# Kernel optimization log

Hardware: AMD Instinct MI355X
Metric: run time of the kernel (lower is better)

Reference implementation:

```python
import jax, jax.numpy as jnp
import numpy as np

B, N, E, D = 32, 144, 127, 512   # batch, seq (forced to 144 by additive PE), embed_size, encoding_size
H, DK, DV = 8, 64, 64            # heads, dim_k, dim_v
F = 32 * D                       # forward_expansion=32 (default)
L = 4                            # num_layers
EPS = 1e-5


def setup_inputs() -> dict:
    key = jax.random.key(0)
    ks = jax.random.split(key, 20)
    s = 0.02
    x = jax.random.normal(ks[0], (B, N, E), jnp.float32)
    # causal mask: True = masked (future positions)
    future_mask = jnp.broadcast_to(jnp.triu(jnp.ones((N, N), bool), k=1), (B, N, N))
    inp = {
        'batch_size': B,
        'x': x,
        'future_mask': future_mask,
        'Wenc': jax.random.normal(ks[1], (E + 1, D), jnp.float32) * s,
        'benc': jnp.zeros((D,), jnp.float32),
        'Wq': jax.random.normal(ks[2], (L, D, H * DK), jnp.float32) * s,
        'Wk': jax.random.normal(ks[3], (L, D, H * DK), jnp.float32) * s,
        'Wv': jax.random.normal(ks[4], (L, D, H * DV), jnp.float32) * s,
        'Wo': jax.random.normal(ks[5], (L, H * DV, D), jnp.float32) * s,
        'bo': jnp.zeros((L, D), jnp.float32),
        'ln1_g': jnp.ones((L, D), jnp.float32), 'ln1_b': jnp.zeros((L, D), jnp.float32),
        'ln2_g': jnp.ones((L, D), jnp.float32), 'ln2_b': jnp.zeros((L, D), jnp.float32),
        'ln3_g': jnp.ones((L, D), jnp.float32), 'ln3_b': jnp.zeros((L, D), jnp.float32),
        'W1': jax.random.normal(ks[6], (L, D, F), jnp.float32) * s,
        'b1': jnp.zeros((L, F), jnp.float32),
        'W2': jax.random.normal(ks[7], (L, F, D), jnp.float32) * s,
        'b2': jnp.zeros((L, D), jnp.float32),
        'Wdec': jax.random.normal(ks[8], (D, E), jnp.float32) * s,
        'bdec': jnp.zeros((E,), jnp.float32),
    }
    return inp


def _layernorm(x, g, b):
    mu = jnp.mean(x, axis=-1, keepdims=True)
    var = jnp.var(x, axis=-1, keepdims=True)
    return (x - mu) * jax.lax.rsqrt(var + EPS) * g + b


def _mha(values_in, keys_in, query_in, mask, Wq, Wk, Wv, Wo, bo):
    b = query_in.shape[0]
    q = (query_in @ Wq).reshape(b, -1, H, DK).transpose(0, 2, 1, 3)   # [b,H,N,DK]
    k = (keys_in @ Wk).reshape(b, -1, H, DK).transpose(0, 2, 1, 3)
    v = (values_in @ Wv).reshape(b, -1, H, DV).transpose(0, 2, 1, 3)  # [b,H,N,DV]
    scores = jnp.einsum('bhnk,bhmk->bhnm', q, k)  # NOTE: no 1/sqrt(dk) scaling in original
    if mask is not None:
        scores = jnp.where(mask[:, None, :, :], jnp.float32(-1e20), scores)
    attn = jax.nn.softmax(scores, axis=-1)
    # torch.einsum('bhnn,bhnv->bhnv') takes the DIAGONAL of attn and scales v elementwise
    diag = jnp.diagonal(attn, axis1=2, axis2=3)  # [b,H,N]
    out = diag[..., None] * v                    # [b,H,N,DV]
    out = out.transpose(0, 2, 1, 3).reshape(b, -1, H * DV)
    return out @ Wo + bo


def reference(batch_size, x, future_mask, Wenc, benc, Wq, Wk, Wv, Wo, bo,
              ln1_g, ln1_b, ln2_g, ln2_b, ln3_g, ln3_b, W1, b1, W2, b2, Wdec, bdec):
    # Additive positional encoding: append arange(N)/max as extra channel
    pe = (jnp.arange(N, dtype=jnp.float32) / jnp.float32(N - 1))[None, :, None]
    xp = jnp.concatenate([x, jnp.broadcast_to(pe, (x.shape[0], N, 1))], axis=2)
    xe = xp @ Wenc + benc  # [B,N,D]
    out = xe
    for l in range(L):
        a = _mha(out, out, out, future_mask, Wq[l], Wk[l], Wv[l], Wo[l], bo[l])
        q = _layernorm(a + xe, ln1_g[l], ln1_b[l])
        a = _mha(xe, xe, q, None, Wq[l], Wk[l], Wv[l], Wo[l], bo[l])
        ff = jax.nn.relu(a @ W1[l] + b1[l]) @ W2[l] + b2[l]
        ao = _layernorm(ff + a, ln2_g[l], ln2_b[l])
        ff2 = jax.nn.relu(ao @ W1[l] + b1[l]) @ W2[l] + b2[l]
        out = _layernorm(ao + ff2, ln3_g[l], ln3_b[l])
    return out @ Wdec + bdec  # [B,N,E]
```

## Files before the change

### kernel.cpp

```cpp
#include <hip/hip_runtime.h>
#include <stdint.h>


typedef unsigned short u16;
typedef unsigned int   u32;
typedef __attribute__((ext_vector_type(8))) short s16x8;
typedef __attribute__((ext_vector_type(4))) float f32x4;

#define AS1 __attribute__((address_space(1)))
#define AS3 __attribute__((address_space(3)))

__device__ __forceinline__ float bf2f(u16 h) { return __uint_as_float(((u32)h) << 16); }
__device__ __forceinline__ u16 f2bf(float f) {
  u32 u = __float_as_uint(f);
  u32 r = (u + 0x7fffu + ((u >> 16) & 1u)) >> 16;
  return (u16)r;
}
__device__ __forceinline__ void gl_lds16(const u16* g, u16* l) {
  __builtin_amdgcn_global_load_lds((const AS1 void*)g, (AS3 void*)l, 16, 0, 0);
}

template<bool BIAS, bool RELU, bool OBF>
__global__ __launch_bounds__(256, 2)
void gemm_bt(const u16* __restrict__ A, int lda,
             const u16* __restrict__ Bt, int ldb,
             void* __restrict__ Cv, int ldc,
             const float* __restrict__ bias,
             int K, int nreal, long long sstride)
{
  __shared__ __align__(16) u16 As[2][128 * 64];
  __shared__ __align__(16) u16 Bs[2][128 * 64];
  const int tid  = threadIdx.x;
  const int wave = tid >> 6, lane = tid & 63;
  const int m0 = blockIdx.x * 128, n0 = blockIdx.y * 128;
  const long long koff = (long long)blockIdx.z * K;
  A  += (size_t)m0 * lda + koff;
  Bt += (size_t)n0 * ldb + koff;

  const int r0 = tid >> 3;
  const int sp = ((tid & 7) ^ (r0 & 7)) * 8;
  const u16* gA = A  + (size_t)r0 * lda + sp;
  const u16* gB = Bt + (size_t)r0 * ldb + sp;
  u16* lA = &As[0][tid * 8];
  u16* lB = &Bs[0][tid * 8];

  const int wr = (wave >> 1) * 64, wc = (wave & 1) * 64;
  const int fr = lane & 15, kq = lane >> 4;
  const int s0 = ((0 * 4 + kq) ^ (fr & 7)) * 8;
  const int s1 = ((1 * 4 + kq) ^ (fr & 7)) * 8;

  f32x4 acc[4][4] = {};
  const int NT = K >> 6;

#pragma unroll
  for (int q = 0; q < 4; ++q) gl_lds16(gA + (size_t)q * 32 * lda, lA + q * 2048);
#pragma unroll
  for (int q = 0; q < 4; ++q) gl_lds16(gB + (size_t)q * 32 * ldb, lB + q * 2048);
  gA += 64; gB += 64;

  for (int t = 0; t < NT; ++t) {
    __syncthreads();
    const int cur = t & 1;
    if (t + 1 < NT) {
      u16* dA = lA + (cur ^ 1) * (128 * 64);
      u16* dB = lB + (cur ^ 1) * (128 * 64);
#pragma unroll
      for (int q = 0; q < 4; ++q) gl_lds16(gA + (size_t)q * 32 * lda, dA + q * 2048);
#pragma unroll
      for (int q = 0; q < 4; ++q) gl_lds16(gB + (size_t)q * 32 * ldb, dB + q * 2048);
      gA += 64; gB += 64;
    }
    const u16* Ab = &As[cur][0];
    const u16* Bb = &Bs[cur][0];
    s16x8 a0[4], a1[4], b0[4], b1[4];
#pragma unroll
    for (int i = 0; i < 4; ++i) {
      const int ra = (wr + i * 16 + fr) * 64;
      a0[i] = *(const s16x8*)&Ab[ra + s0];
      a1[i] = *(const s16x8*)&Ab[ra + s1];
    }
#pragma unroll
    for (int j = 0; j < 4; ++j) {
      const int rb = (wc + j * 16 + fr) * 64;
      b0[j] = *(const s16x8*)&Bb[rb + s0];
      b1[j] = *(const s16x8*)&Bb[rb + s1];
    }
#pragma unroll
    for (int i = 0; i < 4; ++i)
#pragma unroll
      for (int j = 0; j < 4; ++j)
        acc[i][j] = __builtin_amdgcn_mfma_f32_16x16x32_bf16(a0[i], b0[j], acc[i][j], 0, 0, 0);
#pragma unroll
    for (int i = 0; i < 4; ++i)
#pragma unroll
      for (int j = 0; j < 4; ++j)
        acc[i][j] = __builtin_amdgcn_mfma_f32_16x16x32_bf16(a1[i], b1[j], acc[i][j], 0, 0, 0);
  }

#pragma unroll
  for (int j = 0; j < 4; ++j) {
    const int ccol = n0 + wc + j * 16 + fr;
    if (ccol >= nreal) continue;
    const float bv = BIAS ? bias[ccol] : 0.0f;
#pragma unroll
    for (int i = 0; i < 4; ++i) {
#pragma unroll
      for (int r = 0; r < 4; ++r) {
        const int crow = m0 + wr + i * 16 + kq * 4 + r;
        float v = acc[i][j][r] + bv;
        if (RELU) v = fmaxf(v, 0.0f);
        if (OBF) ((u16*)Cv)[(size_t)crow * ldc + ccol] = f2bf(v);
        else ((float*)Cv + (size_t)blockIdx.z * sstride)[(size_t)crow * ldc + ccol] = v;
      }
    }
  }
}

__global__ void tcvt(u16* __restrict__ Wt, const float* __restrict__ W,
                     int K, int N, int Npad)
{
  __shared__ float t[32][33];
  const int n0 = blockIdx.x * 32, k0 = blockIdx.y * 32;
  const int tx = threadIdx.x, ty = threadIdx.y;
#pragma unroll
  for (int i = 0; i < 4; ++i) {
    int k = k0 + ty + i * 8, n = n0 + tx;
    t[ty + i * 8][tx] = (k < K && n < N) ? W[(size_t)k * N + n] : 0.f;
  }
  __syncthreads();
#pragma unroll
  for (int i = 0; i < 4; ++i) {
    int n = n0 + ty + i * 8, k = k0 + tx;
    if (n < Npad) Wt[(size_t)n * K + k] = f2bf(t[tx][ty + i * 8]);
  }
}

template<bool CAUSAL>
__global__ __launch_bounds__(192)
void attn_diag(float* __restrict__ diag,
               const u16* __restrict__ Q, int ldq,
               const u16* __restrict__ Kp, int ldk)
{
  __shared__ float Kl[144][64];
  const int bh = blockIdx.x;
  const int b = bh >> 3, h = bh & 7;
  const int tid = threadIdx.x;

  for (int c = tid; c < 144 * 8; c += 192) {
    int m = c >> 3, c8 = c & 7;
    uint4 u = *(const uint4*)(Kp + (size_t)(b * 144 + m) * ldk + h * 64 + c8 * 8);
    float* dst = &Kl[m][c8 * 8];
    dst[0] = __uint_as_float(u.x << 16); dst[1] = __uint_as_float(u.x & 0xffff0000u);
    dst[2] = __uint_as_float(u.y << 16); dst[3] = __uint_as_float(u.y & 0xffff0000u);
    dst[4] = __uint_as_float(u.z << 16); dst[5] = __uint_as_float(u.z & 0xffff0000u);
    dst[6] = __uint_as_float(u.w << 16); dst[7] = __uint_as_float(u.w & 0xffff0000u);
  }
  __syncthreads();
  if (tid >= 144) return;
  const int n = tid;
  float q[64];
  const uint4* qp = (const uint4*)(Q + (size_t)(b * 144 + n) * ldq + h * 64);
#pragma unroll
  for (int c = 0; c < 8; ++c) {
    uint4 u = qp[c];
    q[c*8+0] = __uint_as_float(u.x << 16); q[c*8+1] = __uint_as_float(u.x & 0xffff0000u);
    q[c*8+2] = __uint_as_float(u.y << 16); q[c*8+3] = __uint_as_float(u.y & 0xffff0000u);
    q[c*8+4] = __uint_as_float(u.z << 16); q[c*8+5] = __uint_as_float(u.z & 0xffff0000u);
    q[c*8+6] = __uint_as_float(u.w << 16); q[c*8+7] = __uint_as_float(u.w & 0xffff0000u);
  }
  const int mmax = CAUSAL ? n : 143;
  float mx = -3.4e38f, sm = 0.f, sdiag = 0.f;
  for (int m = 0; m <= mmax; ++m) {
    float s0 = 0, s1 = 0, s2 = 0, s3 = 0;
#pragma unroll
    for (int c = 0; c < 64; c += 4) {
      s0 = fmaf(q[c + 0], Kl[m][c + 0], s0);
      s1 = fmaf(q[c + 1], Kl[m][c + 1], s1);
      s2 = fmaf(q[c + 2], Kl[m][c + 2], s2);
      s3 = fmaf(q[c + 3], Kl[m][c + 3], s3);
    }
    float s = (s0 + s1) + (s2 + s3);
    if (m == n) sdiag = s;
    float nmx = fmaxf(mx, s);
    sm = sm * __expf(mx - nmx) + __expf(s - nmx);
    mx = nmx;
  }
  diag[(size_t)bh * 144 + n] = __expf(sdiag - mx) / sm;
}

__global__ void scale_v(u16* __restrict__ outb, const float* __restrict__ diag,
                        const u16* __restrict__ V, int ldv)
{
  const int idx = blockIdx.x * 256 + threadIdx.x;
  const int r = idx >> 9, d = idx & 511;
  const int b = r / 144, n = r - b * 144;
  const int h = d >> 6;
  const float dg = diag[((size_t)b * 8 + h) * 144 + n];
  outb[(size_t)r * 512 + d] = f2bf(dg * bf2f(V[(size_t)r * ldv + d]));
}

__global__ __launch_bounds__(128)
void ln_dual(float* __restrict__ outf, u16* __restrict__ outb,
             const float* __restrict__ A, const float* __restrict__ Bv,
             const float* __restrict__ g, const float* __restrict__ be)
{
  const int r = blockIdx.x, t = threadIdx.x;
  float4 a = ((const float4*)(A + (size_t)r * 512))[t];
  float4 b = ((const float4*)(Bv + (size_t)r * 512))[t];
  const float x0 = a.x + b.x, x1 = a.y + b.y, x2 = a.z + b.z, x3 = a.w + b.w;
  float s = x0 + x1 + x2 + x3;
  float q = x0 * x0 + x1 * x1 + x2 * x2 + x3 * x3;
#pragma unroll
  for (int off = 32; off > 0; off >>= 1) { s += __shfl_down(s, off); q += __shfl_down(q, off); }
  __shared__ float ss[2], qs[2];
  if ((t & 63) == 0) { ss[t >> 6] = s; qs[t >> 6] = q; }
  __syncthreads();
  s = ss[0] + ss[1]; q = qs[0] + qs[1];
  const float mean = s * (1.f / 512.f);
  const float var  = q * (1.f / 512.f) - mean * mean;
  const float rs = rsqrtf(var + 1e-5f);
  float4 gg = ((const float4*)g)[t];
  float4 bb = ((const float4*)be)[t];
  const float o0 = (x0 - mean) * rs * gg.x + bb.x;
  const float o1 = (x1 - mean) * rs * gg.y + bb.y;
  const float o2 = (x2 - mean) * rs * gg.z + bb.z;
  const float o3 = (x3 - mean) * rs * gg.w + bb.w;
  if (outf) ((float4*)(outf + (size_t)r * 512))[t] = make_float4(o0, o1, o2, o3);
  if (outb) {
    uint2 u;
    u.x = (u32)f2bf(o0) | ((u32)f2bf(o1) << 16);
    u.y = (u32)f2bf(o2) | ((u32)f2bf(o3) << 16);
    ((uint2*)(outb + (size_t)r * 512))[t] = u;
  }
}

__global__ void f32_to_bf16_vec(u16* __restrict__ o, const float* __restrict__ a)
{
  const int i = blockIdx.x * 256 + threadIdx.x;
  float4 v = ((const float4*)a)[i];
  uint2 u;
  u.x = (u32)f2bf(v.x) | ((u32)f2bf(v.y) << 16);
  u.y = (u32)f2bf(v.z) | ((u32)f2bf(v.w) << 16);
  ((uint2*)o)[i] = u;
}

__global__ void reduce_ff(float* __restrict__ ff, const float* __restrict__ parts,
                          const float* __restrict__ bias)
{
  const int i = blockIdx.x * 256 + threadIdx.x;
  float4 acc = ((const float4*)bias)[i & 127];
#pragma unroll
  for (int s = 0; s < 8; ++s) {
    float4 p = ((const float4*)(parts + (size_t)s * 4608 * 512))[i];
    acc.x += p.x; acc.y += p.y; acc.z += p.z; acc.w += p.w;
  }
  ((float4*)ff)[i] = acc;
}

__global__ void build_xp(u16* __restrict__ xp, const float* __restrict__ x)
{
  const int i = blockIdx.x * 256 + threadIdx.x;
  const int r = i >> 7, e = i & 127;
  const float v = (e < 127) ? x[(size_t)r * 127 + e] : (float)(r % 144) * (1.f / 143.f);
  xp[i] = f2bf(v);
}

extern "C" void kernel_launch(void* const* d_in, const int* in_sizes, int n_in,
                              void* d_out, int out_size, void* d_ws, size_t ws_size,
                              hipStream_t stream)
{
  (void)in_sizes; (void)n_in; (void)out_size; (void)ws_size;
  const float* x    = (const float*)d_in[1];
  const float* Wenc = (const float*)d_in[3];
  const float* benc = (const float*)d_in[4];
  const float* Wq   = (const float*)d_in[5];
  const float* Wk   = (const float*)d_in[6];
  const float* Wv   = (const float*)d_in[7];
  const float* Wo   = (const float*)d_in[8];
  const float* bo   = (const float*)d_in[9];
  const float* ln1g = (const float*)d_in[10];
  const float* ln1b = (const float*)d_in[11];
  const float* ln2g = (const float*)d_in[12];
  const float* ln2b = (const float*)d_in[13];
  const float* ln3g = (const float*)d_in[14];
  const float* ln3b = (const float*)d_in[15];
  const float* W1   = (const float*)d_in[16];
  const float* b1   = (const float*)d_in[17];
  const float* W2   = (const float*)d_in[18];
  const float* b2   = (const float*)d_in[19];
  const float* Wdec = (const float*)d_in[20];
  const float* bdec = (const float*)d_in[21];

  char* w = (char*)d_ws;
  auto alloc = [&](size_t bytes) { void* p = (void*)w; w += (bytes + 255) & ~(size_t)255; return p; };
  u16*   wt_qkv = (u16*)alloc((size_t)1536 * 512 * 2);
  u16*   wt_o   = (u16*)alloc((size_t)512 * 512 * 2);
  u16*   wt_1   = (u16*)alloc((size_t)16384 * 512 * 2);
  u16*   wt_2   = (u16*)alloc((size_t)512 * 16384 * 2);
  u16*   wt_enc = (u16*)alloc((size_t)512 * 128 * 2);
  u16*   wt_dec = (u16*)alloc((size_t)128 * 512 * 2);
  float* xe_f   = (float*)alloc((size_t)4608 * 512 * 4);
  u16*   xe_bf  = (u16*)alloc((size_t)4608 * 512 * 2);
  u16*   out_bf = (u16*)alloc((size_t)4608 * 512 * 2);
  u16*   qkv_bf = (u16*)alloc((size_t)4608 * 1536 * 2);
  float* diag   = (float*)alloc((size_t)256 * 144 * 4);
  u16*   attn_bf= (u16*)alloc((size_t)4608 * 512 * 2);
  float* a1     = (float*)alloc((size_t)4608 * 512 * 4);
  u16*   qln_bf = (u16*)alloc((size_t)4608 * 512 * 2);
  float* a2     = (float*)alloc((size_t)4608 * 512 * 4);
  u16*   a2_bf  = (u16*)alloc((size_t)4608 * 512 * 2);
  u16*   hidden = (u16*)alloc((size_t)4608 * 8192 * 2);
  float* parts  = (float*)alloc((size_t)8 * 4608 * 512 * 4);
  float* ff     = (float*)alloc((size_t)4608 * 512 * 4);
  float* ao_f   = (float*)alloc((size_t)4608 * 512 * 4);
  u16*   ao_bf  = (u16*)alloc((size_t)4608 * 512 * 2);
  float* ff2    = a1;
  u16*   xp_bf  = hidden;

  const long long PSTRIDE = (long long)4608 * 512;

  tcvt<<<dim3(16, 4), dim3(32, 8), 0, stream>>>(wt_enc, Wenc, 128, 512, 512);
  tcvt<<<dim3(4, 16), dim3(32, 8), 0, stream>>>(wt_dec, Wdec, 512, 127, 128);
  build_xp<<<2304, 256, 0, stream>>>(xp_bf, x);
  gemm_bt<true, false, false><<<dim3(36, 4, 1), 256, 0, stream>>>(
      xp_bf, 128, wt_enc, 128, xe_f, 512, benc, 128, 512, 0);
  f32_to_bf16_vec<<<2304, 256, 0, stream>>>(xe_bf, xe_f);

  const u16* in_bf = xe_bf;
  for (int l = 0; l < 4; ++l) {
    const size_t wsz = (size_t)512 * 512;
    tcvt<<<dim3(16, 16), dim3(32, 8), 0, stream>>>(wt_qkv,               Wq + l * wsz, 512, 512, 512);
    tcvt<<<dim3(16, 16), dim3(32, 8), 0, stream>>>(wt_qkv + 512 * 512,   Wk + l * wsz, 512, 512, 512);
    tcvt<<<dim3(16, 16), dim3(32, 8), 0, stream>>>(wt_qkv + 1024 * 512,  Wv + l * wsz, 512, 512, 512);
    tcvt<<<dim3(16, 16), dim3(32, 8), 0, stream>>>(wt_o, Wo + l * wsz, 512, 512, 512);
    tcvt<<<dim3(512, 16), dim3(32, 8), 0, stream>>>(wt_1, W1 + (size_t)l * 512 * 16384, 512, 16384, 16384);
    tcvt<<<dim3(16, 512), dim3(32, 8), 0, stream>>>(wt_2, W2 + (size_t)l * 16384 * 512, 16384, 512, 512);

    gemm_bt<false, false, true><<<dim3(36, 12, 1), 256, 0, stream>>>(
        in_bf, 512, wt_qkv, 512, qkv_bf, 1536, nullptr, 512, 1536, 0);
    attn_diag<true><<<256, 192, 0, stream>>>(diag, qkv_bf, 1536, qkv_bf + 512, 1536);
    scale_v<<<9216, 256, 0, stream>>>(attn_bf, diag, qkv_bf + 1024, 1536);
    gemm_bt<true, false, false><<<dim3(36, 4, 1), 256, 0, stream>>>(
        attn_bf, 512, wt_o, 512, a1, 512, bo + l * 512, 512, 512, 0);
    ln_dual<<<4608, 128, 0, stream>>>(nullptr, qln_bf, a1, xe_f, ln1g + l * 512, ln1b + l * 512);

    gemm_bt<false, false, true><<<dim3(36, 4, 1), 256, 0, stream>>>(
        qln_bf, 512, wt_qkv, 512, attn_bf, 512, nullptr, 512, 512, 0);
    gemm_bt<false, false, true><<<dim3(36, 8, 1), 256, 0, stream>>>(
        xe_bf, 512, wt_qkv + 512 * 512, 512, qkv_bf, 1024, nullptr, 512, 1024, 0);
    attn_diag<false><<<256, 192, 0, stream>>>(diag, attn_bf, 512, qkv_bf, 1024);
    scale_v<<<9216, 256, 0, stream>>>(attn_bf, diag, qkv_bf + 512, 1024);
    gemm_bt<true, false, false><<<dim3(36, 4, 1), 256, 0, stream>>>(
        attn_bf, 512, wt_o, 512, a2, 512, bo + l * 512, 512, 512, 0);
    f32_to_bf16_vec<<<2304, 256, 0, stream>>>(a2_bf, a2);

    for (int c = 0; c < 2; ++c) {
      gemm_bt<true, true, true><<<dim3(36, 64, 1), 256, 0, stream>>>(
          a2_bf, 512, wt_1 + (size_t)c * 8192 * 512, 512, hidden, 8192,
          b1 + l * 16384 + c * 8192, 512, 8192, 0);
      gemm_bt<false, false, false><<<dim3(36, 4, 4), 256, 0, stream>>>(
          hidden, 8192, wt_2 + c * 8192, 16384,
          parts + (size_t)c * 4 * 4608 * 512, 512, nullptr, 2048, 512, PSTRIDE);
    }
    reduce_ff<<<2304, 256, 0, stream>>>(ff, parts, b2 + l * 512);
    ln_dual<<<4608, 128, 0, stream>>>(ao_f, ao_bf, ff, a2, ln2g + l * 512, ln2b + l * 512);

    for (int c = 0; c < 2; ++c) {
      gemm_bt<true, true, true><<<dim3(36, 64, 1), 256, 0, stream>>>(
          ao_bf, 512, wt_1 + (size_t)c * 8192 * 512, 512, hidden, 8192,
          b1 + l * 16384 + c * 8192, 512, 8192, 0);
      gemm_bt<false, false, false><<<dim3(36, 4, 4), 256, 0, stream>>>(
          hidden, 8192, wt_2 + c * 8192, 16384,
          parts + (size_t)c * 4 * 4608 * 512, 512, nullptr, 2048, 512, PSTRIDE);
    }
    reduce_ff<<<2304, 256, 0, stream>>>(ff2, parts, b2 + l * 512);
    ln_dual<<<4608, 128, 0, stream>>>(nullptr, out_bf, ao_f, ff2, ln3g + l * 512, ln3b + l * 512);
    in_bf = out_bf;
  }

  gemm_bt<true, false, false><<<dim3(36, 1, 1), 256, 0, stream>>>(
      in_bf, 512, wt_dec, 512, (float*)d_out, 127, bdec, 512, 127, 0);
}
```

Before: 3.368 ms.

## Add 256x256-tile triple-buffered GEMM for FFN with XCD-aware block remap

```diff
diff --git a/kernel.cpp b/kernel.cpp
--- a/kernel.cpp
+++ b/kernel.cpp
@@ -18,6 +18,115 @@
 }
 __device__ __forceinline__ void gl_lds16(const u16* g, u16* l) {
   __builtin_amdgcn_global_load_lds((const AS1 void*)g, (AS3 void*)l, 16, 0, 0);
+}
+
+template<bool BIAS, bool RELU, bool OBF, bool XCD>
+__global__ __launch_bounds__(512, 2)
+void gemm256(const u16* __restrict__ A, int lda,
+             const u16* __restrict__ Bt, int ldb,
+             void* __restrict__ Cv, int ldc,
+             const float* __restrict__ bias,
+             int K, long long sstride, int mtiles)
+{
+  __shared__ __align__(16) u16 L[3][2][256 * 32];
+  const int tid  = threadIdx.x;
+  const int wave = tid >> 6, lane = tid & 63;
+
+  int bid = blockIdx.x;
+  if (XCD) {
+    const int cpx = gridDim.x >> 3;
+    bid = (bid & 7) * cpx + (bid >> 3);
+  }
+  const int mt = bid % mtiles, nt = bid / mtiles;
+  const int m0 = mt * 256, n0 = nt * 256;
+  const long long koff = (long long)blockIdx.z * K;
+  A  += (size_t)m0 * lda + koff;
+  Bt += (size_t)n0 * ldb + koff;
+
+  const int row0 = tid >> 2;
+  const int kq_s = (tid & 3) ^ ((row0 >> 1) & 3);
+  const size_t offA0 = (size_t)row0 * lda + kq_s * 8;
+  const size_t offA1 = offA0 + (size_t)128 * lda;
+  const size_t offB0 = (size_t)row0 * ldb + kq_s * 8;
+  const size_t offB1 = offB0 + (size_t)128 * ldb;
+
+  const int wr = (wave >> 2) * 128, wc = (wave & 3) * 64;
+  const int fr = lane & 15, kqe = lane >> 4;
+  const int skq = kqe ^ ((fr >> 1) & 3);
+
+  f32x4 acc[8][4] = {};
+  const int NT = K >> 5;
+
+  {
+    const u16* Ak = A;            const u16* Bk = Bt;
+    gl_lds16(Ak + offA0, &L[0][0][tid * 8]);
+    gl_lds16(Ak + offA1, &L[0][0][tid * 8 + 4096]);
+    gl_lds16(Bk + offB0, &L[0][1][tid * 8]);
+    gl_lds16(Bk + offB1, &L[0][1][tid * 8 + 4096]);
+    Ak += 32; Bk += 32;
+    gl_lds16(Ak + offA0, &L[1][0][tid * 8]);
+    gl_lds16(Ak + offA1, &L[1][0][tid * 8 + 4096]);
+    gl_lds16(Bk + offB0, &L[1][1][tid * 8]);
+    gl_lds16(Bk + offB1, &L[1][1][tid * 8 + 4096]);
+  }
+
+  int cur = 0, pre = 2;
+  for (int t = 0; t < NT; ++t) {
+    if (t + 1 < NT) asm volatile("s_waitcnt vmcnt(4)" ::: "memory");
+    else            asm volatile("s_waitcnt vmcnt(0)" ::: "memory");
+    __builtin_amdgcn_s_barrier();
+    __builtin_amdgcn_sched_barrier(0);
+
+    if (t + 2 < NT) {
+      const u16* Ak = A + (size_t)(t + 2) * 32;
+      const u16* Bk = Bt + (size_t)(t + 2) * 32;
+      u16* sA = &L[pre][0][0];
+      u16* sB = &L[pre][1][0];
+      gl_lds16(Ak + offA0, sA + tid * 8);
+      gl_lds16(Ak + offA1, sA + tid * 8 + 4096);
+      gl_lds16(Bk + offB0, sB + tid * 8);
+      gl_lds16(Bk + offB1, sB + tid * 8 + 4096);
+    }
+
+    const u16* Ab = &L[cur][0][0];
+    const u16* Bb = &L[cur][1][0];
+    s16x8 af[8], bf[4];
+#pragma unroll
+    for (int i = 0; i < 8; ++i)
+      af[i] = *(const s16x8*)&Ab[((wr + i * 16 + fr) * 4 + skq) * 8];
+#pragma unroll
+    for (int j = 0; j < 4; ++j)
+      bf[j] = *(const s16x8*)&Bb[((wc + j * 16 + fr) * 4 + skq) * 8];
+
+    __builtin_amdgcn_s_setprio(1);
+#pragma unroll
+    for (int i = 0; i < 8; ++i)
+#pragma unroll
+      for (int j = 0; j < 4; ++j)
+        acc[i][j] = __builtin_amdgcn_mfma_f32_16x16x32_bf16(af[i], bf[j], acc[i][j], 0, 0, 0);
+    __builtin_amdgcn_s_setprio(0);
+    __builtin_amdgcn_sched_barrier(0);
+
+    cur = (cur == 2) ? 0 : cur + 1;
+    pre = (pre == 2) ? 0 : pre + 1;
+  }
+
+#pragma unroll
+  for (int j = 0; j < 4; ++j) {
+    const int ccol = n0 + wc + j * 16 + fr;
+    const float bv = BIAS ? bias[ccol] : 0.0f;
+#pragma unroll
+    for (int i = 0; i < 8; ++i) {
+#pragma unroll
+      for (int r = 0; r < 4; ++r) {
+        const int crow = m0 + wr + i * 16 + kqe * 4 + r;
+        float v = acc[i][j][r] + bv;
+        if (RELU) v = fmaxf(v, 0.0f);
+        if (OBF) ((u16*)Cv)[(size_t)crow * ldc + ccol] = f2bf(v);
+        else ((float*)Cv + (size_t)blockIdx.z * sstride)[(size_t)crow * ldc + ccol] = v;
+      }
+    }
+  }
 }
 
 template<bool BIAS, bool RELU, bool OBF>
@@ -309,7 +418,7 @@
   u16*   qln_bf = (u16*)alloc((size_t)4608 * 512 * 2);
   float* a2     = (float*)alloc((size_t)4608 * 512 * 4);
   u16*   a2_bf  = (u16*)alloc((size_t)4608 * 512 * 2);
-  u16*   hidden = (u16*)alloc((size_t)4608 * 8192 * 2);
+  u16*   hidden = (u16*)alloc((size_t)4608 * 16384 * 2);
   float* parts  = (float*)alloc((size_t)8 * 4608 * 512 * 4);
   float* ff     = (float*)alloc((size_t)4608 * 512 * 4);
   float* ao_f   = (float*)alloc((size_t)4608 * 512 * 4);
@@ -354,25 +463,17 @@
         attn_bf, 512, wt_o, 512, a2, 512, bo + l * 512, 512, 512, 0);
     f32_to_bf16_vec<<<2304, 256, 0, stream>>>(a2_bf, a2);
 
-    for (int c = 0; c < 2; ++c) {
-      gemm_bt<true, true, true><<<dim3(36, 64, 1), 256, 0, stream>>>(
-          a2_bf, 512, wt_1 + (size_t)c * 8192 * 512, 512, hidden, 8192,
-          b1 + l * 16384 + c * 8192, 512, 8192, 0);
-      gemm_bt<false, false, false><<<dim3(36, 4, 4), 256, 0, stream>>>(
-          hidden, 8192, wt_2 + c * 8192, 16384,
-          parts + (size_t)c * 4 * 4608 * 512, 512, nullptr, 2048, 512, PSTRIDE);
-    }
+    gemm256<true, true, true, true><<<dim3(1152, 1, 1), 512, 0, stream>>>(
+        a2_bf, 512, wt_1, 512, hidden, 16384, b1 + l * 16384, 512, 0, 18);
+    gemm256<false, false, false, false><<<dim3(36, 1, 8), 512, 0, stream>>>(
+        hidden, 16384, wt_2, 16384, parts, 512, nullptr, 2048, PSTRIDE, 18);
     reduce_ff<<<2304, 256, 0, stream>>>(ff, parts, b2 + l * 512);
     ln_dual<<<4608, 128, 0, stream>>>(ao_f, ao_bf, ff, a2, ln2g + l * 512, ln2b + l * 512);
 
-    for (int c = 0; c < 2; ++c) {
-      gemm_bt<true, true, true><<<dim3(36, 64, 1), 256, 0, stream>>>(
-          ao_bf, 512, wt_1 + (size_t)c * 8192 * 512, 512, hidden, 8192,
-          b1 + l * 16384 + c * 8192, 512, 8192, 0);
-      gemm_bt<false, false, false><<<dim3(36, 4, 4), 256, 0, stream>>>(
-          hidden, 8192, wt_2 + c * 8192, 16384,
-          parts + (size_t)c * 4 * 4608 * 512, 512, nullptr, 2048, 512, PSTRIDE);
-    }
+    gemm256<true, true, true, true><<<dim3(1152, 1, 1), 512, 0, stream>>>(
+        ao_bf, 512, wt_1, 512, hidden, 16384, b1 + l * 16384, 512, 0, 18);
+    gemm256<false, false, false, false><<<dim3(36, 1, 8), 512, 0, stream>>>(
+        hidden, 16384, wt_2, 16384, parts, 512, nullptr, 2048, PSTRIDE, 18);
     reduce_ff<<<2304, 256, 0, stream>>>(ff2, parts, b2 + l * 512);
     ln_dual<<<4608, 128, 0, stream>>>(nullptr, out_bf, ao_f, ff2, ln3g + l * 512, ln3b + l * 512);
     in_bf = out_bf;
```

Result: slower. 3.530 ms (+4.8%).
